# Performance work log

Hardware: AMD Instinct MI355X
Metric: run time of the kernel (lower is better)

## Reference

```python
import jax, jax.numpy as jnp
import numpy as np

HIDDEN = 128
POOL = 64
G = 4            # grid_size
NBHD = 2.0       # neighborhood_size (meters)
NUM_SCENES = 256
PEDS = 64        # pedestrians per scene (uniform seq_start_end)


def setup_inputs() -> dict:
    key = jax.random.key(0)
    k1, k2, k3 = jax.random.split(key, 3)
    hidden_states = jax.random.normal(k1, (NUM_SCENES * PEDS, HIDDEN), jnp.float32)
    positions = jax.random.uniform(k2, (NUM_SCENES * PEDS, 2), jnp.float32)
    fan_in = HIDDEN * G * G
    weight = jax.random.normal(k3, (fan_in, POOL), jnp.float32) / np.sqrt(fan_in)
    bias = jnp.zeros((POOL,), jnp.float32)
    return {
        "hidden_states": hidden_states,
        "positions": positions,
        "weight": weight,
        "bias": bias,
        "peds_per_scene": PEDS,
    }


def reference(hidden_states, positions, weight, bias, peds_per_scene):
    total, H = hidden_states.shape
    P = peds_per_scene
    B = total // P
    h = hidden_states.reshape(B, P, H)
    p = positions.reshape(B, P, 2)

    # rel[b, i, j] = pos[j] - pos[i]  (matches curr_pos - curr_pos[i:i+1])
    rel = p[:, None, :, :] - p[:, :, None, :]            # [B, P, P, 2]
    in_range = (jnp.abs(rel[..., 0]) <= NBHD) & (jnp.abs(rel[..., 1]) <= NBHD)
    not_self = ~jnp.eye(P, dtype=bool)[None]
    mask = in_range & not_self                            # [B, P, P]

    # int() truncation == floor here since (rel + NBHD) >= 0 inside the range check
    scale = G / (2.0 * NBHD)
    gx = jnp.clip(jnp.floor((rel[..., 0] + NBHD) * scale).astype(jnp.int32), 0, G - 1)
    gy = jnp.clip(jnp.floor((rel[..., 1] + NBHD) * scale).astype(jnp.int32), 0, G - 1)
    grid_idx = gy * G + gx                                # [B, P, P]

    # scatter-add of neighbor hidden states into G*G bins via masked one-hot
    onehot = jax.nn.one_hot(grid_idx, G * G, dtype=h.dtype) * mask[..., None].astype(h.dtype)
    grid = jnp.einsum('bijg,bjh->bigh', onehot, h)        # [B, P, G*G, H]

    flat = grid.reshape(B * P, G * G * H)                 # row-major: (grid_idx, hidden)
    return flat @ weight + bias                            # [total_peds, POOL]
```

## Files before the change

kernel.cpp:

```cpp
#include <hip/hip_runtime.h>
#include <cstdint>

#define PEDS   64
#define HIDDEN 128
#define POOL   64
#define GRIDG  4
#define NBHD   2.0f

typedef unsigned short u16;
typedef unsigned int   u32;
typedef __attribute__((ext_vector_type(8))) short bf16x8;
typedef __attribute__((ext_vector_type(4))) float f32x4;

__device__ __forceinline__ u16 f2bf(float f) {
    u32 u = __float_as_uint(f);
    u += 0x7fffu + ((u >> 16) & 1u);
    return (u16)(u >> 16);
}
__device__ __forceinline__ u32 pack2bf(float a, float b) {
    return (u32)f2bf(a) | ((u32)f2bf(b) << 16);
}

__global__ __launch_bounds__(256) void prep_kernel(
    const float* __restrict__ h, const float* __restrict__ w,
    u16* __restrict__ hB, u16* __restrict__ wB, int hb_threads)
{
    int t = blockIdx.x * 256 + threadIdx.x;
    if (t < hb_threads) {
        int lane = t & 63, st4 = (t >> 6) & 3, mt = (t >> 8) & 3, scene = t >> 10;
        int row = scene * 64 + mt * 16 + (lane & 15);
        int k0  = st4 * 32 + (lane >> 4) * 8;
        const float4* s = (const float4*)(h + (size_t)row * HIDDEN + k0);
        float4 f0 = s[0], f1 = s[1];
        *(uint4*)(hB + (size_t)t * 8) = make_uint4(
            pack2bf(f0.x, f0.y), pack2bf(f0.z, f0.w),
            pack2bf(f1.x, f1.y), pack2bf(f1.z, f1.w));
    } else {
        int u = t - hb_threads;
        if (u < 16 * 4 * 4 * 64) {
            int lane = u & 63, st4 = (u >> 6) & 3, cg = (u >> 8) & 3, g = u >> 10;
            int c  = cg * 16 + (lane & 15);
            int k0 = st4 * 32 + (lane >> 4) * 8;
            const float* s = w + ((size_t)g * HIDDEN + k0) * POOL + c;
            float v[8];
#pragma unroll
            for (int e = 0; e < 8; ++e) v[e] = s[(size_t)e * POOL];
            *(uint4*)(wB + (size_t)u * 8) = make_uint4(
                pack2bf(v[0], v[1]), pack2bf(v[2], v[3]),
                pack2bf(v[4], v[5]), pack2bf(v[6], v[7]));
        }
    }
}

__global__ __launch_bounds__(256) void social_main(
    const u16* __restrict__ hB, const u16* __restrict__ wB,
    const float* __restrict__ pos, const float* __restrict__ bias,
    float* __restrict__ out)
{
    __shared__ u32 wmask[4];
    __shared__ u16 hwT[32 * 256];

    const int tid  = threadIdx.x;
    const int mt   = tid >> 6;
    const int lane = tid & 63;
    const int l15  = lane & 15;
    const int q    = lane >> 4;
    const int scene = blockIdx.x >> 1;
    const int ch    = blockIdx.x & 1;

    bf16x8 af[4];
    const u16* hfb = hB + (((size_t)scene * 4 + mt) * 4) * 512;
#pragma unroll
    for (int st4 = 0; st4 < 4; ++st4)
        af[st4] = *(const bf16x8*)(hfb + st4 * 512 + lane * 8);

    const float bv0 = bias[ch * 32 + l15];
    const float bv1 = bias[ch * 32 + 16 + l15];

    float2 pp = ((const float2*)pos)[(size_t)scene * PEDS + lane];
    const int i = mt * 16 + l15;
    const float pxi = __shfl(pp.x, i), pyi = __shfl(pp.y, i);
    const float scale = (float)GRIDG / (2.0f * NBHD);
    u32 gpk[4] = {0u, 0u, 0u, 0u};
    u32 um = 0u;
#pragma unroll
    for (int jh = 0; jh < 2; ++jh) {
#pragma unroll
        for (int u8 = 0; u8 < 8; ++u8) {
            int j = jh * 32 + q * 8 + u8;
            float rx = __shfl(pp.x, j) - pxi;
            float ry = __shfl(pp.y, j) - pyi;
            u32 gb = 0xffu;
            if ((i != j) && (fabsf(rx) <= NBHD) && (fabsf(ry) <= NBHD)) {
                int gx = (int)floorf((rx + NBHD) * scale); gx = min(max(gx, 0), GRIDG - 1);
                int gy = (int)floorf((ry + NBHD) * scale); gy = min(max(gy, 0), GRIDG - 1);
                gb = (u32)(gy * GRIDG + gx);
                um |= 1u << gb;
            }
            gpk[jh * 2 + (u8 >> 2)] |= gb << ((u8 & 3) * 8);
        }
    }
#pragma unroll
    for (int off = 32; off; off >>= 1) um |= __shfl_xor(um, off);
    if (lane == 0) wmask[mt] = um;
    __syncthreads();

    u32 mask = wmask[0] | wmask[1] | wmask[2] | wmask[3];
    mask = __builtin_amdgcn_readfirstlane(mask);

    f32x4 oacc0 = (f32x4){0.f, 0.f, 0.f, 0.f};
    f32x4 oacc1 = (f32x4){0.f, 0.f, 0.f, 0.f};
    u32 rem = mask;

    while (true) {
        int gs[4];
#pragma unroll
        for (int t = 0; t < 4; ++t) {
            gs[t] = rem ? (__ffs(rem) - 1) : -1;
            if (rem) rem &= rem - 1u;
        }

#pragma unroll
        for (int t = 0; t < 4; ++t) {
            int ge = gs[t] < 0 ? 0 : gs[t];
            const u16* wf0 = wB + (((size_t)ge * 4 + ch * 2 + 0) * 4) * 512;
            const u16* wf1 = wB + (((size_t)ge * 4 + ch * 2 + 1) * 4) * 512;
            f32x4 a10 = (f32x4){0.f, 0.f, 0.f, 0.f};
            f32x4 a11 = (f32x4){0.f, 0.f, 0.f, 0.f};
#pragma unroll
            for (int st4 = 0; st4 < 4; ++st4) {
                bf16x8 b0 = *(const bf16x8*)(wf0 + st4 * 512 + lane * 8);
                bf16x8 b1 = *(const bf16x8*)(wf1 + st4 * 512 + lane * 8);
                a10 = __builtin_amdgcn_mfma_f32_16x16x32_bf16(af[st4], b0, a10, 0, 0, 0);
                a11 = __builtin_amdgcn_mfma_f32_16x16x32_bf16(af[st4], b1, a11, 0, 0, 0);
            }
            int ci = t * 8 + mt * 2 + (q >> 1);
#pragma unroll
            for (int ni = 0; ni < 2; ++ni) {
                const f32x4& a = ni ? a11 : a10;
                int cr  = ni * 16 + l15;
                int ci2 = (ci & 0x10) | ((ci & 15) ^ l15);
                *(uint2*)&hwT[cr * 256 + ci2 * 8 + (q & 1) * 4] =
                    make_uint2(pack2bf(a[0], a[1]), pack2bf(a[2], a[3]));
            }
        }
        __syncthreads();

#pragma unroll
        for (int step = 0; step < 8; ++step) {
            int slot = step >> 1, jh = step & 1;
            int gt = gs[slot];
            u32 wa = gpk[jh * 2], wb = gpk[jh * 2 + 1];
            union { u16 hx[8]; bf16x8 v; } mu;
#pragma unroll
            for (int b = 0; b < 4; ++b)
                mu.hx[b]     = (((wa >> (b * 8)) & 0xffu) == (u32)gt) ? (u16)0x3F80 : (u16)0;
#pragma unroll
            for (int b = 0; b < 4; ++b)
                mu.hx[4 + b] = (((wb >> (b * 8)) & 0xffu) == (u32)gt) ? (u16)0x3F80 : (u16)0;
            int ci = step * 4 + q;
#pragma unroll
            for (int ni = 0; ni < 2; ++ni) {
                int cr  = ni * 16 + l15;
                int ci2 = (ci & 0x10) | ((ci & 15) ^ l15);
                bf16x8 bb = *(const bf16x8*)&hwT[cr * 256 + ci2 * 8];
                if (ni == 0)
                    oacc0 = __builtin_amdgcn_mfma_f32_16x16x32_bf16(mu.v, bb, oacc0, 0, 0, 0);
                else
                    oacc1 = __builtin_amdgcn_mfma_f32_16x16x32_bf16(mu.v, bb, oacc1, 0, 0, 0);
            }
        }
        if (!rem) break;
        __syncthreads();
    }

    size_t ob = ((size_t)scene * PEDS + mt * 16 + q * 4) * POOL + ch * 32 + l15;
#pragma unroll
    for (int r = 0; r < 4; ++r) {
        out[ob + (size_t)r * POOL]      = oacc0[r] + bv0;
        out[ob + (size_t)r * POOL + 16] = oacc1[r] + bv1;
    }
}

extern "C" void kernel_launch(void* const* d_in, const int* in_sizes, int n_in,
                              void* d_out, int out_size, void* d_ws, size_t ws_size,
                              hipStream_t stream) {
    const float* h    = (const float*)d_in[0];
    const float* pos  = (const float*)d_in[1];
    const float* w    = (const float*)d_in[2];
    const float* bias = (const float*)d_in[3];
    float* out = (float*)d_out;

    const int total = in_sizes[0] / HIDDEN;
    const int B     = total / PEDS;

    u16* hB = (u16*)d_ws;
    u16* wB = hB + (size_t)total * HIDDEN;

    const int hb_threads = total * 16;
    const int wb_threads = 16 * 4 * 4 * 64;
    const int prep_blocks = (hb_threads + wb_threads + 255) / 256;

    hipLaunchKernelGGL(prep_kernel, dim3(prep_blocks), dim3(256), 0, stream,
                       h, w, hB, wB, hb_threads);
    hipLaunchKernelGGL(social_main, dim3(B * 2), dim3(256), 0, stream,
                       hB, wB, pos, bias, out);
}
```

Baseline: 75.20 us.

## Fuse bf16 prep into single-pass kernel with per-wave register-resident projection

Removes the separate bf16 conversion kernel and the shared-memory staging. Each wave now loads all 64 scene rows of fp32 hidden state and converts them to bf16 in registers. It reads the fp32 weight slice for each occupied grid cell, prefetching the next cell, and chains the projection MFMA output directly into the one-hot aggregation MFMA without __syncthreads. This drops one launch, the intermediate global writes and the block barriers. In exchange each wave redundantly computes the full 64-row projection, register pressure rises (64-float prefetch buffer, 16 A fragments, 8 accumulators), and each block re-reads and re-converts fp32 weights with strided loads.

```diff
diff --git a/kernel.cpp b/kernel.cpp
--- a/kernel.cpp
+++ b/kernel.cpp
@@ -21,45 +21,11 @@
     return (u32)f2bf(a) | ((u32)f2bf(b) << 16);
 }
 
-__global__ __launch_bounds__(256) void prep_kernel(
-    const float* __restrict__ h, const float* __restrict__ w,
-    u16* __restrict__ hB, u16* __restrict__ wB, int hb_threads)
-{
-    int t = blockIdx.x * 256 + threadIdx.x;
-    if (t < hb_threads) {
-        int lane = t & 63, st4 = (t >> 6) & 3, mt = (t >> 8) & 3, scene = t >> 10;
-        int row = scene * 64 + mt * 16 + (lane & 15);
-        int k0  = st4 * 32 + (lane >> 4) * 8;
-        const float4* s = (const float4*)(h + (size_t)row * HIDDEN + k0);
-        float4 f0 = s[0], f1 = s[1];
-        *(uint4*)(hB + (size_t)t * 8) = make_uint4(
-            pack2bf(f0.x, f0.y), pack2bf(f0.z, f0.w),
-            pack2bf(f1.x, f1.y), pack2bf(f1.z, f1.w));
-    } else {
-        int u = t - hb_threads;
-        if (u < 16 * 4 * 4 * 64) {
-            int lane = u & 63, st4 = (u >> 6) & 3, cg = (u >> 8) & 3, g = u >> 10;
-            int c  = cg * 16 + (lane & 15);
-            int k0 = st4 * 32 + (lane >> 4) * 8;
-            const float* s = w + ((size_t)g * HIDDEN + k0) * POOL + c;
-            float v[8];
-#pragma unroll
-            for (int e = 0; e < 8; ++e) v[e] = s[(size_t)e * POOL];
-            *(uint4*)(wB + (size_t)u * 8) = make_uint4(
-                pack2bf(v[0], v[1]), pack2bf(v[2], v[3]),
-                pack2bf(v[4], v[5]), pack2bf(v[6], v[7]));
-        }
-    }
-}
-
-__global__ __launch_bounds__(256) void social_main(
-    const u16* __restrict__ hB, const u16* __restrict__ wB,
-    const float* __restrict__ pos, const float* __restrict__ bias,
+__global__ __launch_bounds__(256, 2) void social_onepass(
+    const float* __restrict__ h, const float* __restrict__ pos,
+    const float* __restrict__ w, const float* __restrict__ bias,
     float* __restrict__ out)
 {
-    __shared__ u32 wmask[4];
-    __shared__ u16 hwT[32 * 256];
-
     const int tid  = threadIdx.x;
     const int mt   = tid >> 6;
     const int lane = tid & 63;
@@ -68,26 +34,18 @@
     const int scene = blockIdx.x >> 1;
     const int ch    = blockIdx.x & 1;
 
-    bf16x8 af[4];
-    const u16* hfb = hB + (((size_t)scene * 4 + mt) * 4) * 512;
-#pragma unroll
-    for (int st4 = 0; st4 < 4; ++st4)
-        af[st4] = *(const bf16x8*)(hfb + st4 * 512 + lane * 8);
+    float2 pp = ((const float2*)pos)[(size_t)scene * PEDS + lane];
 
-    const float bv0 = bias[ch * 32 + l15];
-    const float bv1 = bias[ch * 32 + 16 + l15];
-
-    float2 pp = ((const float2*)pos)[(size_t)scene * PEDS + lane];
     const int i = mt * 16 + l15;
     const float pxi = __shfl(pp.x, i), pyi = __shfl(pp.y, i);
     const float scale = (float)GRIDG / (2.0f * NBHD);
     u32 gpk[4] = {0u, 0u, 0u, 0u};
     u32 um = 0u;
 #pragma unroll
-    for (int jh = 0; jh < 2; ++jh) {
+    for (int kk = 0; kk < 2; ++kk) {
 #pragma unroll
-        for (int u8 = 0; u8 < 8; ++u8) {
-            int j = jh * 32 + q * 8 + u8;
+        for (int e = 0; e < 8; ++e) {
+            int j = kk * 32 + q * 8 + e;
             float rx = __shfl(pp.x, j) - pxi;
             float ry = __shfl(pp.y, j) - pyi;
             u32 gb = 0xffu;
@@ -97,81 +55,117 @@
                 gb = (u32)(gy * GRIDG + gx);
                 um |= 1u << gb;
             }
-            gpk[jh * 2 + (u8 >> 2)] |= gb << ((u8 & 3) * 8);
+            gpk[kk * 2 + (e >> 2)] |= gb << ((e & 3) * 8);
         }
     }
 #pragma unroll
     for (int off = 32; off; off >>= 1) um |= __shfl_xor(um, off);
-    if (lane == 0) wmask[mt] = um;
-    __syncthreads();
+    um = __builtin_amdgcn_readfirstlane(um);
 
-    u32 mask = wmask[0] | wmask[1] | wmask[2] | wmask[3];
-    mask = __builtin_amdgcn_readfirstlane(mask);
+    const float* hbase = h + (size_t)scene * (PEDS * HIDDEN);
+    const int jrow = (l15 >> 2) * 8 + (l15 & 3);
+    bf16x8 af[16];
+#pragma unroll
+    for (int mtile = 0; mtile < 4; ++mtile) {
+        int jr = (mtile >> 1) * 32 + (mtile & 1) * 4 + jrow;
+        const float* rp = hbase + (size_t)jr * HIDDEN + q * 8;
+#pragma unroll
+        for (int st4 = 0; st4 < 4; ++st4) {
+            float4 f0 = *(const float4*)(rp + st4 * 32);
+            float4 f1 = *(const float4*)(rp + st4 * 32 + 4);
+            union { u32 u[4]; bf16x8 v; } uu;
+            uu.u[0] = pack2bf(f0.x, f0.y);
+            uu.u[1] = pack2bf(f0.z, f0.w);
+            uu.u[2] = pack2bf(f1.x, f1.y);
+            uu.u[3] = pack2bf(f1.z, f1.w);
+            af[mtile * 4 + st4] = uu.v;
+        }
+    }
 
+    const float bv0 = bias[ch * 32 + l15];
+    const float bv1 = bias[ch * 32 + 16 + l15];
     f32x4 oacc0 = (f32x4){0.f, 0.f, 0.f, 0.f};
     f32x4 oacc1 = (f32x4){0.f, 0.f, 0.f, 0.f};
-    u32 rem = mask;
 
-    while (true) {
-        int gs[4];
+    const int ng = __popc(um);
+    u32 rem = um;
+    int g = 0;
+    float wf32[64];
+    const float* wb = w + ch * 32 + l15;
+    if (ng) {
+        g = __ffs(rem) - 1; rem &= rem - 1u;
 #pragma unroll
-        for (int t = 0; t < 4; ++t) {
-            gs[t] = rem ? (__ffs(rem) - 1) : -1;
-            if (rem) rem &= rem - 1u;
+        for (int f = 0; f < 8; ++f) {
+            int ni = f >> 2, st4 = f & 3;
+            const float* src = wb + ((size_t)(g * HIDDEN + st4 * 32 + q * 8)) * POOL + ni * 16;
+#pragma unroll
+            for (int e = 0; e < 8; ++e) wf32[f * 8 + e] = src[(size_t)e * POOL];
+        }
+    }
+
+    for (int t = 0; t < ng; ++t) {
+        bf16x8 wfrag[8];
+#pragma unroll
+        for (int f = 0; f < 8; ++f) {
+            union { u32 u[4]; bf16x8 v; } uu;
+            uu.u[0] = pack2bf(wf32[f * 8 + 0], wf32[f * 8 + 1]);
+            uu.u[1] = pack2bf(wf32[f * 8 + 2], wf32[f * 8 + 3]);
+            uu.u[2] = pack2bf(wf32[f * 8 + 4], wf32[f * 8 + 5]);
+            uu.u[3] = pack2bf(wf32[f * 8 + 6], wf32[f * 8 + 7]);
+            wfrag[f] = uu.v;
+        }
+        const int gcur = g;
+        if (rem) {
+            g = __ffs(rem) - 1; rem &= rem - 1u;
+#pragma unroll
+            for (int f = 0; f < 8; ++f) {
+                int ni = f >> 2, st4 = f & 3;
+                const float* src = wb + ((size_t)(g * HIDDEN + st4 * 32 + q * 8)) * POOL + ni * 16;
+#pragma unroll
+                for (int e = 0; e < 8; ++e) wf32[f * 8 + e] = src[(size_t)e * POOL];
+            }
+        }
+
+        f32x4 acc1[4][2];
+#pragma unroll
+        for (int a = 0; a < 4; ++a) {
+            acc1[a][0] = (f32x4){0.f, 0.f, 0.f, 0.f};
+            acc1[a][1] = (f32x4){0.f, 0.f, 0.f, 0.f};
+        }
+#pragma unroll
+        for (int st4 = 0; st4 < 4; ++st4) {
+#pragma unroll
+            for (int mtile = 0; mtile < 4; ++mtile) {
+                acc1[mtile][0] = __builtin_amdgcn_mfma_f32_16x16x32_bf16(
+                    af[mtile * 4 + st4], wfrag[st4], acc1[mtile][0], 0, 0, 0);
+                acc1[mtile][1] = __builtin_amdgcn_mfma_f32_16x16x32_bf16(
+                    af[mtile * 4 + st4], wfrag[4 + st4], acc1[mtile][1], 0, 0, 0);
+            }
         }
 
 #pragma unroll
-        for (int t = 0; t < 4; ++t) {
-            int ge = gs[t] < 0 ? 0 : gs[t];
-            const u16* wf0 = wB + (((size_t)ge * 4 + ch * 2 + 0) * 4) * 512;
-            const u16* wf1 = wB + (((size_t)ge * 4 + ch * 2 + 1) * 4) * 512;
-            f32x4 a10 = (f32x4){0.f, 0.f, 0.f, 0.f};
-            f32x4 a11 = (f32x4){0.f, 0.f, 0.f, 0.f};
-#pragma unroll
-            for (int st4 = 0; st4 < 4; ++st4) {
-                bf16x8 b0 = *(const bf16x8*)(wf0 + st4 * 512 + lane * 8);
-                bf16x8 b1 = *(const bf16x8*)(wf1 + st4 * 512 + lane * 8);
-                a10 = __builtin_amdgcn_mfma_f32_16x16x32_bf16(af[st4], b0, a10, 0, 0, 0);
-                a11 = __builtin_amdgcn_mfma_f32_16x16x32_bf16(af[st4], b1, a11, 0, 0, 0);
-            }
-            int ci = t * 8 + mt * 2 + (q >> 1);
-#pragma unroll
-            for (int ni = 0; ni < 2; ++ni) {
-                const f32x4& a = ni ? a11 : a10;
-                int cr  = ni * 16 + l15;
-                int ci2 = (ci & 0x10) | ((ci & 15) ^ l15);
-                *(uint2*)&hwT[cr * 256 + ci2 * 8 + (q & 1) * 4] =
-                    make_uint2(pack2bf(a[0], a[1]), pack2bf(a[2], a[3]));
-            }
-        }
-        __syncthreads();
-
-#pragma unroll
-        for (int step = 0; step < 8; ++step) {
-            int slot = step >> 1, jh = step & 1;
-            int gt = gs[slot];
-            u32 wa = gpk[jh * 2], wb = gpk[jh * 2 + 1];
+        for (int kk = 0; kk < 2; ++kk) {
+            u32 wa = gpk[kk * 2], wc = gpk[kk * 2 + 1];
             union { u16 hx[8]; bf16x8 v; } mu;
 #pragma unroll
             for (int b = 0; b < 4; ++b)
-                mu.hx[b]     = (((wa >> (b * 8)) & 0xffu) == (u32)gt) ? (u16)0x3F80 : (u16)0;
+                mu.hx[b]     = (((wa >> (b * 8)) & 0xffu) == (u32)gcur) ? (u16)0x3F80 : (u16)0;
 #pragma unroll
             for (int b = 0; b < 4; ++b)
-                mu.hx[4 + b] = (((wb >> (b * 8)) & 0xffu) == (u32)gt) ? (u16)0x3F80 : (u16)0;
-            int ci = step * 4 + q;
+                mu.hx[4 + b] = (((wc >> (b * 8)) & 0xffu) == (u32)gcur) ? (u16)0x3F80 : (u16)0;
 #pragma unroll
             for (int ni = 0; ni < 2; ++ni) {
-                int cr  = ni * 16 + l15;
-                int ci2 = (ci & 0x10) | ((ci & 15) ^ l15);
-                bf16x8 bb = *(const bf16x8*)&hwT[cr * 256 + ci2 * 8];
+                union { u32 u[4]; bf16x8 v; } bb;
+                bb.u[0] = pack2bf(acc1[kk * 2][ni][0],     acc1[kk * 2][ni][1]);
+                bb.u[1] = pack2bf(acc1[kk * 2][ni][2],     acc1[kk * 2][ni][3]);
+                bb.u[2] = pack2bf(acc1[kk * 2 + 1][ni][0], acc1[kk * 2 + 1][ni][1]);
+                bb.u[3] = pack2bf(acc1[kk * 2 + 1][ni][2], acc1[kk * 2 + 1][ni][3]);
                 if (ni == 0)
-                    oacc0 = __builtin_amdgcn_mfma_f32_16x16x32_bf16(mu.v, bb, oacc0, 0, 0, 0);
+                    oacc0 = __builtin_amdgcn_mfma_f32_16x16x32_bf16(mu.v, bb.v, oacc0, 0, 0, 0);
                 else
-                    oacc1 = __builtin_amdgcn_mfma_f32_16x16x32_bf16(mu.v, bb, oacc1, 0, 0, 0);
+                    oacc1 = __builtin_amdgcn_mfma_f32_16x16x32_bf16(mu.v, bb.v, oacc1, 0, 0, 0);
             }
         }
-        if (!rem) break;
-        __syncthreads();
     }
 
     size_t ob = ((size_t)scene * PEDS + mt * 16 + q * 4) * POOL + ch * 32 + l15;
@@ -194,15 +188,6 @@
     const int total = in_sizes[0] / HIDDEN;
     const int B     = total / PEDS;
 
-    u16* hB = (u16*)d_ws;
-    u16* wB = hB + (size_t)total * HIDDEN;
-
-    const int hb_threads = total * 16;
-    const int wb_threads = 16 * 4 * 4 * 64;
-    const int prep_blocks = (hb_threads + wb_threads + 255) / 256;
-
-    hipLaunchKernelGGL(prep_kernel, dim3(prep_blocks), dim3(256), 0, stream,
-                       h, w, hB, wB, hb_threads);
-    hipLaunchKernelGGL(social_main, dim3(B * 2), dim3(256), 0, stream,
-                       hB, wB, pos, bias, out);
+    hipLaunchKernelGGL(social_onepass, dim3(B * 2), dim3(256), 0, stream,
+                       h, pos, w, bias, out);
 }
```

Measured after the change: 82.74 us. 1.1x slower.
